# Kernel tuning notes

Hardware: AMD Instinct MI355X
Metric: run time of the kernel (lower is better)

Reference implementation:

```python
import jax, jax.numpy as jnp
import numpy as np

HEAD_SIZE = 128  # embeddings_dims // no_of_heads = 4096 // 32


def apply_rope(v):
    # v: [B, S, d] with d = HEAD_SIZE; interleaved-pair rotation as in source
    B, S, d = v.shape
    pos = jnp.arange(S, dtype=jnp.float32)[:, None]              # [S, 1]
    idx = jnp.arange(0, d, 2, dtype=jnp.float32)[None, :]        # [1, d//2]
    theta = jnp.power(10000.0, -2.0 * idx / d)                   # [1, d//2]
    angles = pos * theta                                         # [S, d//2]
    cos = jnp.cos(angles)
    sin = jnp.sin(angles)
    vr = v.reshape(B, S, d // 2, 2)
    x0, x1 = vr[..., 0], vr[..., 1]
    out = jnp.stack([x0 * cos - x1 * sin, x1 * cos + x0 * sin], axis=-1)
    return out.reshape(B, S, d)


def setup_inputs() -> dict:
    key = jax.random.key(0)
    kx, kq, kk, kv = jax.random.split(key, 4)
    B, S, D = 2, 4096, 4096
    d = HEAD_SIZE
    scale = 1.0 / np.sqrt(D)
    return {
        "x": jax.random.normal(kx, (B, S, D), dtype=jnp.float32),
        "Wq": jax.random.normal(kq, (d, D), dtype=jnp.float32) * scale,
        "Wk": jax.random.normal(kk, (d, D), dtype=jnp.float32) * scale,
        "Wv": jax.random.normal(kv, (d, D), dtype=jnp.float32) * scale,
    }


def reference(x, Wq, Wk, Wv):
    # single attention head, non-flash path (eval mode: dropout = identity)
    B, S, D = x.shape
    q = jnp.einsum('bsd,hd->bsh', x, Wq)  # [B, S, head]
    k = jnp.einsum('bsd,hd->bsh', x, Wk)
    v = jnp.einsum('bsd,hd->bsh', x, Wv)
    q = apply_rope(q)
    k = apply_rope(k)
    scale = k.shape[-1] ** (-0.5)
    scores = jnp.einsum('bqh,bkh->bqk', q, k) * scale  # [B, S, S]
    causal = jnp.tril(jnp.ones((S, S), dtype=bool))
    scores = jnp.where(causal, scores, -jnp.inf)
    weights = jax.nn.softmax(scores, axis=-1)
    out = jnp.einsum('bqk,bkh->bqh', weights, v)  # [B, S, head]
    return out
```

## Files before the change

### kernel.cpp

```cpp
#include <hip/hip_runtime.h>

typedef _Float16 half8 __attribute__((ext_vector_type(8)));
typedef _Float16 half2v __attribute__((ext_vector_type(2)));
typedef float f32x4 __attribute__((ext_vector_type(4)));

#define S_LEN 4096
#define D_DIM 4096
#define HD 128


__device__ __forceinline__ void gload_lds16(const _Float16* g, _Float16* l) {
    __builtin_amdgcn_global_load_lds(
        (const __attribute__((address_space(1))) unsigned int*)g,
        (__attribute__((address_space(3))) unsigned int*)l, 16, 0, 0);
}

__global__ __launch_bounds__(256) void convw_kernel(const float* __restrict__ wq,
                                                    const float* __restrict__ wk,
                                                    const float* __restrict__ wv,
                                                    _Float16* __restrict__ wh) {
    const int g = blockIdx.x * 256 + threadIdx.x;
    const int p = g >> 16;
    const int off = (g & 65535) * 8;
    const float* src = ((p == 0) ? wq : (p == 1) ? wk : wv) + off;
    float4 v0 = *(const float4*)src;
    float4 v1 = *(const float4*)(src + 4);
    half8 h = { (_Float16)v0.x, (_Float16)v0.y, (_Float16)v0.z, (_Float16)v0.w,
                (_Float16)v1.x, (_Float16)v1.y, (_Float16)v1.z, (_Float16)v1.w };
    *(half8*)&wh[(size_t)p * 524288 + off] = h;
}

#define QSTR 136
template<int KSPLIT>
__global__ __launch_bounds__(256) void proj_kernel(const float* __restrict__ x,
                                                   const _Float16* __restrict__ wh,
                                                   _Float16* __restrict__ qw,
                                                   _Float16* __restrict__ kw,
                                                   _Float16* __restrict__ vt,
                                                   float* __restrict__ P) {
    __shared__ __align__(16) _Float16 smem[17408];
    const int tid = threadIdx.x;
    const int wg = blockIdx.x;
    const int nwg = 384 * KSPLIT;
    const int swz = (wg & 7) * (nwg >> 3) + (wg >> 3);
    const int bx = swz % 3;
    const int rest = swz / 3;
    const int ks = (KSPLIT == 2) ? (rest & 1) : 0;
    const int M0 = ((KSPLIT == 2) ? (rest >> 1) : rest) * 64;
    const int NS = 128 / KSPLIT;
    const int lane = tid & 63, wv_ = tid >> 6;
    const int l15 = lane & 15, quad = lane >> 4;

    const int arow = tid >> 2, acol = (tid & 3) * 8;
    const float* xa = x + (size_t)(M0 + arow) * D_DIM + acol + ks * (D_DIM / 2);
    const _Float16* wsrc = wh + (size_t)bx * 128 * D_DIM + ks * (D_DIM / 2) +
                           (size_t)(wv_ * 32 + l15) * D_DIM + quad * 8;

    const int awoff = ((arow >> 4) * 64 + (arow & 15) + (tid & 3) * 16) * 8;
    const int rdoff = lane * 8;

    f32x4 acc[4][2];
    for (int mi = 0; mi < 4; ++mi)
        for (int ni = 0; ni < 2; ++ni)
            acc[mi][ni] = (f32x4){0.f, 0.f, 0.f, 0.f};

    auto stageA = [&](_Float16* buf, float4 A0, float4 A1) {
        half8 ha = { (_Float16)A0.x, (_Float16)A0.y, (_Float16)A0.z, (_Float16)A0.w,
                     (_Float16)A1.x, (_Float16)A1.y, (_Float16)A1.z, (_Float16)A1.w };
        *(half8*)&buf[awoff] = ha;
    };
    auto stageB = [&](_Float16* buf, int slab) {
        const _Float16* s = wsrc + slab * 32;
        gload_lds16(s,               &buf[2048 + wv_ * 1024]);
        gload_lds16(s + 16 * D_DIM,  &buf[2048 + wv_ * 1024 + 512]);
    };
    auto compute = [&](const _Float16* buf) {
        const _Float16* Af = buf + rdoff;
        const _Float16* Bf = buf + 2048 + wv_ * 1024 + rdoff;
        half8 af[4], bf[2];
        for (int mi = 0; mi < 4; ++mi)
            af[mi] = *(const half8*)(Af + mi * 512);
        for (int ni = 0; ni < 2; ++ni)
            bf[ni] = *(const half8*)(Bf + ni * 512);
        for (int mi = 0; mi < 4; ++mi)
            for (int ni = 0; ni < 2; ++ni)
                acc[mi][ni] = __builtin_amdgcn_mfma_f32_16x16x32_f16(af[mi], bf[ni],
                                                                     acc[mi][ni], 0, 0, 0);
    };

    float4 a0_0, a0_1, a1_0, a1_1;
    a0_0 = *(const float4*)(xa);      a0_1 = *(const float4*)(xa + 4);
    a1_0 = *(const float4*)(xa + 32); a1_1 = *(const float4*)(xa + 36);
    stageB(smem, 0);

    for (int i = 0; i < NS; i += 2) {
        stageA(smem, a0_0, a0_1);
        __syncthreads();
        if (i + 2 < NS) {
            a0_0 = *(const float4*)(xa + (i + 2) * 32);
            a0_1 = *(const float4*)(xa + (i + 2) * 32 + 4);
        }
        stageB(smem + 6144, i + 1);
        compute(smem);
        stageA(smem + 6144, a1_0, a1_1);
        __syncthreads();
        if (i + 3 < NS) {
            a1_0 = *(const float4*)(xa + (i + 3) * 32);
            a1_1 = *(const float4*)(xa + (i + 3) * 32 + 4);
        }
        if (i + 2 < NS) stageB(smem, i + 2);
        compute(smem + 6144);
    }
    __syncthreads();

    if (KSPLIT == 2) {
        float* sf = (float*)smem;
        for (int mi = 0; mi < 4; ++mi)
            for (int ni = 0; ni < 2; ++ni)
                for (int r = 0; r < 4; ++r)
                    sf[(mi * 16 + quad * 4 + r) * 132 + wv_ * 32 + ni * 16 + l15] =
                        acc[mi][ni][r];
        __syncthreads();
        const int row = tid >> 2, c0 = (tid & 3) * 32;
        float* dst = P + ((size_t)(ks * 3 + bx) * 8192 + M0 + row) * HD + c0;
        for (int j = 0; j < 8; ++j)
            *(float4*)(dst + j * 4) = *(const float4*)&sf[row * 132 + c0 + j * 4];
    } else if (bx < 2) {
        for (int mi = 0; mi < 4; ++mi)
            for (int ni = 0; ni < 2; ++ni)
                for (int r = 0; r < 4; ++r)
                    smem[(mi * 16 + quad * 4 + r) * QSTR + wv_ * 32 + ni * 16 + l15] =
                        (_Float16)acc[mi][ni][r];
        __syncthreads();
        _Float16* dst = ((bx == 0) ? qw : kw) + (size_t)M0 * HD;
        const int row = tid >> 2, c0 = (tid & 3) * 32;
        for (int j = 0; j < 4; ++j)
            *(half8*)&dst[row * HD + c0 + j * 8] = *(const half8*)&smem[row * QSTR + c0 + j * 8];
    } else {
        for (int mi = 0; mi < 4; ++mi)
            for (int ni = 0; ni < 2; ++ni)
                for (int r = 0; r < 4; ++r)
                    smem[(wv_ * 32 + ni * 16 + l15) * QSTR + mi * 16 + quad * 4 + r] =
                        (_Float16)acc[mi][ni][r];
        __syncthreads();
        _Float16* dst = vt + (size_t)(M0 >> 12) * HD * S_LEN + (M0 & (S_LEN - 1));
        const int hd = tid >> 1, s0 = (tid & 1) * 32;
        for (int j = 0; j < 4; ++j)
            *(half8*)&dst[(size_t)hd * S_LEN + s0 + j * 8] =
                *(const half8*)&smem[hd * QSTR + s0 + j * 8];
    }
}

__global__ __launch_bounds__(256) void combine_kernel(const float* __restrict__ P,
                                                      _Float16* __restrict__ qw,
                                                      _Float16* __restrict__ kw,
                                                      _Float16* __restrict__ vt) {
    const int tid = threadIdx.x;
    const int M0 = blockIdx.x * 64;
    const int row = tid >> 2, c0 = (tid & 3) * 32;
    if (blockIdx.y == 0) {
        const float* Pq0 = P + ((size_t)0 * 8192 + M0 + row) * HD + c0;
        const float* Pq1 = P + ((size_t)3 * 8192 + M0 + row) * HD + c0;
        const float* Pk0 = P + ((size_t)1 * 8192 + M0 + row) * HD + c0;
        const float* Pk1 = P + ((size_t)4 * 8192 + M0 + row) * HD + c0;
        float qv[32], kv[32];
#pragma unroll
        for (int j = 0; j < 8; ++j) {
            float4 a = *(const float4*)(Pq0 + j * 4);
            float4 b = *(const float4*)(Pq1 + j * 4);
            float4 c = *(const float4*)(Pk0 + j * 4);
            float4 d = *(const float4*)(Pk1 + j * 4);
            qv[j * 4 + 0] = a.x + b.x; qv[j * 4 + 1] = a.y + b.y;
            qv[j * 4 + 2] = a.z + b.z; qv[j * 4 + 3] = a.w + b.w;
            kv[j * 4 + 0] = c.x + d.x; kv[j * 4 + 1] = c.y + d.y;
            kv[j * 4 + 2] = c.z + d.z; kv[j * 4 + 3] = c.w + d.w;
        }
        const int s = (M0 + row) & (S_LEN - 1);
        half8 oq[4], ok[4];
#pragma unroll
        for (int jp = 0; jp < 16; ++jp) {
            const int pi = (c0 >> 1) + jp;
            const float theta = exp2f((float)pi * -0.4152410118609203f);
            float sn, cn;
            sincosf((float)s * theta, &sn, &cn);
            const float q0 = qv[2 * jp], q1 = qv[2 * jp + 1];
            const float k0 = kv[2 * jp], k1 = kv[2 * jp + 1];
            oq[jp >> 2][(2 * jp) & 7]     = (_Float16)(q0 * cn - q1 * sn);
            oq[jp >> 2][(2 * jp + 1) & 7] = (_Float16)(q1 * cn + q0 * sn);
            ok[jp >> 2][(2 * jp) & 7]     = (_Float16)(k0 * cn - k1 * sn);
            ok[jp >> 2][(2 * jp + 1) & 7] = (_Float16)(k1 * cn + k0 * sn);
        }
        _Float16* qdst = qw + (size_t)(M0 + row) * HD + c0;
        _Float16* kdst = kw + (size_t)(M0 + row) * HD + c0;
#pragma unroll
        for (int j = 0; j < 4; ++j) {
            *(half8*)(qdst + j * 8) = oq[j];
            *(half8*)(kdst + j * 8) = ok[j];
        }
    } else {
        __shared__ __align__(16) _Float16 sh[128][72];
        const float* Pv0 = P + ((size_t)2 * 8192 + M0 + row) * HD + c0;
        const float* Pv1 = P + ((size_t)5 * 8192 + M0 + row) * HD + c0;
#pragma unroll
        for (int j = 0; j < 8; ++j) {
            float4 a = *(const float4*)(Pv0 + j * 4);
            float4 b = *(const float4*)(Pv1 + j * 4);
            sh[c0 + j * 4 + 0][row] = (_Float16)(a.x + b.x);
            sh[c0 + j * 4 + 1][row] = (_Float16)(a.y + b.y);
            sh[c0 + j * 4 + 2][row] = (_Float16)(a.z + b.z);
            sh[c0 + j * 4 + 3][row] = (_Float16)(a.w + b.w);
        }
        __syncthreads();
        const int hd = tid >> 1, s0 = (tid & 1) * 32;
        _Float16* dst = vt + (size_t)(M0 >> 12) * HD * S_LEN + (size_t)hd * S_LEN +
                        (M0 & (S_LEN - 1)) + s0;
        for (int j = 0; j < 4; ++j)
            *(half8*)(dst + j * 8) = *(const half8*)&sh[hd][s0 + j * 8];
    }
}

__global__ __launch_bounds__(256) void rope_kernel(_Float16* __restrict__ qw,
                                                   _Float16* __restrict__ kw) {
    const int g = blockIdx.x * 256 + threadIdx.x;
    const int m = g >> 6, p = g & 63;
    const int s = m & (S_LEN - 1);
    const float theta = exp2f((float)p * -0.4152410118609203f);
    float sn, cn;
    sincosf((float)s * theta, &sn, &cn);
    const size_t off = (size_t)m * HD + 2 * p;
    half2v qv = *(half2v*)&qw[off];
    half2v kv = *(half2v*)&kw[off];
    float q0 = qv[0], q1 = qv[1], k0 = kv[0], k1 = kv[1];
    half2v qo = { (_Float16)(q0 * cn - q1 * sn), (_Float16)(q1 * cn + q0 * sn) };
    half2v ko = { (_Float16)(k0 * cn - k1 * sn), (_Float16)(k1 * cn + k0 * sn) };
    *(half2v*)&qw[off] = qo;
    *(half2v*)&kw[off] = ko;
}

__device__ __forceinline__ void load_kf(const _Float16* __restrict__ kb, int kbase,
                                        int l15, int quad, half8* kf) {
    const _Float16* kr = kb + (size_t)(kbase + l15) * HD + quad * 8;
    for (int kk = 0; kk < 4; ++kk) {
        kf[kk]     = *(const half8*)(kr + kk * 32);
        kf[4 + kk] = *(const half8*)(kr + 16 * HD + kk * 32);
    }
}

template<bool MASKED>
__device__ __forceinline__ void attn_tile(int kbase, int qg, int l15, int quad,
                                          const half8* kf,
                                          const _Float16* __restrict__ vtb,
                                          const half8* bq, f32x4* acc,
                                          float& mrun, float& lrun) {
    const float csc = 0.1275174348796053f;
    half8 va[8];
    const _Float16* vr = vtb + (size_t)l15 * S_LEN + kbase + quad * 8;
    for (int c = 0; c < 8; ++c)
        va[c] = *(const half8*)(vr + (size_t)c * 16 * S_LEN);
    f32x4 st0 = (f32x4){0.f, 0.f, 0.f, 0.f};
    f32x4 st1 = (f32x4){0.f, 0.f, 0.f, 0.f};
    for (int kk = 0; kk < 4; ++kk) {
        st0 = __builtin_amdgcn_mfma_f32_16x16x32_f16(kf[kk],     bq[kk], st0, 0, 0, 0);
        st1 = __builtin_amdgcn_mfma_f32_16x16x32_f16(kf[4 + kk], bq[kk], st1, 0, 0, 0);
    }
    float p0[4], p1[4];
    float mloc = -1e30f;
    for (int r = 0; r < 4; ++r) {
        float v0 = st0[r] * csc;
        float v1 = st1[r] * csc;
        if (MASKED) {
            const int key0 = kbase + quad * 4 + r;
            if (key0 > qg)      v0 = -1e30f;
            if (key0 + 16 > qg) v1 = -1e30f;
        }
        p0[r] = v0; p1[r] = v1;
        mloc = fmaxf(mloc, fmaxf(v0, v1));
    }
    mloc = fmaxf(mloc, __shfl_xor(mloc, 16));
    mloc = fmaxf(mloc, __shfl_xor(mloc, 32));
    const float mnew = fmaxf(mrun, mloc);
    const float alpha = exp2f(mrun - mnew);
    mrun = mnew;
    float ls = 0.f;
    for (int r = 0; r < 4; ++r) {
        p0[r] = exp2f(p0[r] - mnew);
        p1[r] = exp2f(p1[r] - mnew);
        ls += p0[r] + p1[r];
    }
    ls += __shfl_xor(ls, 16);
    ls += __shfl_xor(ls, 32);
    lrun = lrun * alpha + ls;
    for (int c = 0; c < 8; ++c)
        acc[c] *= alpha;
    int ph0 = __builtin_bit_cast(int, __builtin_amdgcn_cvt_pkrtz(p0[0], p0[1]));
    int ph1 = __builtin_bit_cast(int, __builtin_amdgcn_cvt_pkrtz(p0[2], p0[3]));
    int ph2 = __builtin_bit_cast(int, __builtin_amdgcn_cvt_pkrtz(p1[0], p1[1]));
    int ph3 = __builtin_bit_cast(int, __builtin_amdgcn_cvt_pkrtz(p1[2], p1[3]));
    const int s0 = (l15 + (((quad << 1)    ) & 3) * 16) * 4;
    const int s1 = (l15 + (((quad << 1) + 1) & 3) * 16) * 4;
    int a0 = __builtin_amdgcn_ds_bpermute(s0, ph0);
    int a1 = __builtin_amdgcn_ds_bpermute(s0, ph1);
    int a2 = __builtin_amdgcn_ds_bpermute(s1, ph0);
    int a3 = __builtin_amdgcn_ds_bpermute(s1, ph1);
    int b0 = __builtin_amdgcn_ds_bpermute(s0, ph2);
    int b1 = __builtin_amdgcn_ds_bpermute(s0, ph3);
    int b2 = __builtin_amdgcn_ds_bpermute(s1, ph2);
    int b3 = __builtin_amdgcn_ds_bpermute(s1, ph3);
    const bool lo = quad < 2;
    int4 pi = { lo ? a0 : b0, lo ? a1 : b1, lo ? a2 : b2, lo ? a3 : b3 };
    half8 pf = __builtin_bit_cast(half8, pi);
    for (int c = 0; c < 8; ++c)
        acc[c] = __builtin_amdgcn_mfma_f32_16x16x32_f16(va[c], pf, acc[c], 0, 0, 0);
}

__global__ __launch_bounds__(256) void attn_kernel(const _Float16* __restrict__ q,
                                                   const _Float16* __restrict__ k,
                                                   const _Float16* __restrict__ vt,
                                                   float* __restrict__ out) {
    __shared__ __align__(16) float Osh[4][16][132];
    __shared__ float msh[4][16];
    __shared__ float lsh[4][16];
    const int tid = threadIdx.x;
    const int lane = tid & 63, wv_ = tid >> 6;
    const int l15 = lane & 15, quad = lane >> 4;
    const int bidx = blockIdx.x;
    const int b = bidx & 1;
    const int t = 255 - (bidx >> 1);
    const int qb = t * 16;
    const int qg = qb + l15;

    const _Float16* qp = q + (size_t)(b * S_LEN + qb) * HD;
    half8 bq[4];
    for (int kk = 0; kk < 4; ++kk)
        bq[kk] = *(const half8*)&qp[l15 * HD + kk * 32 + quad * 8];

    f32x4 acc[8];
    for (int c = 0; c < 8; ++c) acc[c] = (f32x4){0.f, 0.f, 0.f, 0.f};
    float mrun = -1e30f, lrun = 0.f;

    const _Float16* kb = k + (size_t)b * S_LEN * HD;
    const _Float16* vtb = vt + (size_t)b * HD * S_LEN;

    const int nfull = (qb + 1) >> 5;
    const int kend = nfull * 32;
    const bool hasm = ((nfull & 3) == wv_);
    const int kb0 = wv_ * 32;

    half8 kf[8], kf2[8];
    if (kb0 < kend)      load_kf(kb, kb0, l15, quad, kf);
    else if (hasm)       load_kf(kb, kend, l15, quad, kf);
    for (int kbase = kb0; kbase < kend; kbase += 128) {
        const int kn = kbase + 128;
        if (kn < kend)   load_kf(kb, kn, l15, quad, kf2);
        else if (hasm)   load_kf(kb, kend, l15, quad, kf2);
        attn_tile<false>(kbase, qg, l15, quad, kf, vtb, bq, acc, mrun, lrun);
        for (int j = 0; j < 8; ++j) kf[j] = kf2[j];
    }
    if (hasm)
        attn_tile<true>(kend, qg, l15, quad, kf, vtb, bq, acc, mrun, lrun);

    for (int c = 0; c < 8; ++c)
        *(f32x4*)&Osh[wv_][l15][c * 16 + quad * 4] = acc[c];
    if (quad == 0) { msh[wv_][l15] = mrun; lsh[wv_][l15] = lrun; }
    __syncthreads();

    const int qr = tid >> 4, dg = (tid & 15) * 8;
    float m0 = msh[0][qr], m1 = msh[1][qr], m2 = msh[2][qr], m3 = msh[3][qr];
    float mm = fmaxf(fmaxf(m0, m1), fmaxf(m2, m3));
    float f0 = exp2f(m0 - mm), f1 = exp2f(m1 - mm), f2 = exp2f(m2 - mm), f3 = exp2f(m3 - mm);
    float l = lsh[0][qr] * f0 + lsh[1][qr] * f1 + lsh[2][qr] * f2 + lsh[3][qr] * f3;
    f32x4 oa = (f32x4){0.f, 0.f, 0.f, 0.f}, ob = oa;
    oa += *(f32x4*)&Osh[0][qr][dg] * f0;  ob += *(f32x4*)&Osh[0][qr][dg + 4] * f0;
    oa += *(f32x4*)&Osh[1][qr][dg] * f1;  ob += *(f32x4*)&Osh[1][qr][dg + 4] * f1;
    oa += *(f32x4*)&Osh[2][qr][dg] * f2;  ob += *(f32x4*)&Osh[2][qr][dg + 4] * f2;
    oa += *(f32x4*)&Osh[3][qr][dg] * f3;  ob += *(f32x4*)&Osh[3][qr][dg + 4] * f3;
    const float inv = 1.0f / l;
    float* op = out + (size_t)(b * S_LEN + qb + qr) * HD + dg;
    *(float4*)op       = (float4){oa[0] * inv, oa[1] * inv, oa[2] * inv, oa[3] * inv};
    *(float4*)(op + 4) = (float4){ob[0] * inv, ob[1] * inv, ob[2] * inv, ob[3] * inv};
}

extern "C" void kernel_launch(void* const* d_in, const int* in_sizes, int n_in,
                              void* d_out, int out_size, void* d_ws, size_t ws_size,
                              hipStream_t stream) {
    const float* x  = (const float*)d_in[0];
    const float* Wq = (const float*)d_in[1];
    const float* Wk = (const float*)d_in[2];
    const float* Wv = (const float*)d_in[3];
    float* out = (float*)d_out;
    char* ws = (char*)d_ws;
    _Float16* qw = (_Float16*)(ws);
    _Float16* kw = (_Float16*)(ws + (2u << 20));
    _Float16* vt = (_Float16*)(ws + (4u << 20));
    _Float16* wh = (_Float16*)(ws + (6u << 20));
    float* P = (float*)(ws + (9u << 20));

    const size_t need2 = (size_t)(9u << 20) + (size_t)2 * 3 * 8192 * 128 * 4;
    convw_kernel<<<dim3(768), dim3(256), 0, stream>>>(Wq, Wk, Wv, wh);
    if (ws_size >= need2) {
        proj_kernel<2><<<dim3(768), dim3(256), 0, stream>>>(x, wh, qw, kw, vt, P);
        combine_kernel<<<dim3(128, 2), dim3(256), 0, stream>>>(P, qw, kw, vt);
    } else {
        proj_kernel<1><<<dim3(384), dim3(256), 0, stream>>>(x, wh, qw, kw, vt, P);
        rope_kernel<<<dim3(2048), dim3(256), 0, stream>>>(qw, kw);
    }
    attn_kernel<<<dim3(512), dim3(256), 0, stream>>>(qw, kw, vt, out);
}
```

Measured before the change: 343.4 us.

## Pre-convert x to fp16 and use direct-to-LDS projection GEMM

Adds a kernel that converts x and the weights to fp16 in one pass, then a new projection kernel that loads both A and B tiles with global-to-LDS async loads, double-buffered, with 64-wide k steps. This removes register-based fp32 loading and conversion of x inside the GEMM. In exchange it adds an extra full pass over x (read fp32, write fp16) and needs a larger workspace; it falls back to the old path otherwise.

Result: slower. 373.4 us (+8.7%).

```diff
diff --git a/kernel.cpp b/kernel.cpp
--- a/kernel.cpp
+++ b/kernel.cpp
@@ -13,6 +13,33 @@
     __builtin_amdgcn_global_load_lds(
         (const __attribute__((address_space(1))) unsigned int*)g,
         (__attribute__((address_space(3))) unsigned int*)l, 16, 0, 0);
+}
+
+__global__ __launch_bounds__(256) void convx_kernel(const float* __restrict__ x,
+                                                    const float* __restrict__ wq,
+                                                    const float* __restrict__ wk,
+                                                    const float* __restrict__ wv,
+                                                    _Float16* __restrict__ xh,
+                                                    _Float16* __restrict__ wh) {
+    const int g = blockIdx.x * 256 + threadIdx.x;
+    const float* src;
+    _Float16* dst;
+    if (g < 4194304) {
+        const int off = g * 8;
+        src = x + off;
+        dst = xh + off;
+    } else {
+        const int h = g - 4194304;
+        const int p = h >> 16;
+        const int off = (h & 65535) * 8;
+        src = ((p == 0) ? wq : (p == 1) ? wk : wv) + off;
+        dst = wh + (size_t)p * 524288 + off;
+    }
+    float4 v0 = *(const float4*)src;
+    float4 v1 = *(const float4*)(src + 4);
+    half8 hv = { (_Float16)v0.x, (_Float16)v0.y, (_Float16)v0.z, (_Float16)v0.w,
+                 (_Float16)v1.x, (_Float16)v1.y, (_Float16)v1.z, (_Float16)v1.w };
+    *(half8*)dst = hv;
 }
 
 __global__ __launch_bounds__(256) void convw_kernel(const float* __restrict__ wq,
@@ -28,6 +55,77 @@
     half8 h = { (_Float16)v0.x, (_Float16)v0.y, (_Float16)v0.z, (_Float16)v0.w,
                 (_Float16)v1.x, (_Float16)v1.y, (_Float16)v1.z, (_Float16)v1.w };
     *(half8*)&wh[(size_t)p * 524288 + off] = h;
+}
+
+__global__ __launch_bounds__(256) void projd_kernel(const _Float16* __restrict__ xh,
+                                                    const _Float16* __restrict__ wh,
+                                                    float* __restrict__ P) {
+    __shared__ __align__(16) _Float16 smem[24576];
+    const int tid = threadIdx.x;
+    const int wg = blockIdx.x;
+    const int swz = (wg & 7) * 96 + (wg >> 3);
+    const int bx = swz % 3;
+    const int rest = swz / 3;
+    const int ks = rest & 1;
+    const int M0 = (rest >> 1) * 64;
+    const int lane = tid & 63, wv_ = tid >> 6;
+    const int l15 = lane & 15, quad = lane >> 4;
+
+    const _Float16* asrc = xh + (size_t)(M0 + wv_ * 16 + l15) * D_DIM + ks * (D_DIM / 2) + quad * 8;
+    const _Float16* bsrc = wh + (size_t)bx * 524288 +
+                           (size_t)(wv_ * 32 + l15) * D_DIM + ks * (D_DIM / 2) + quad * 8;
+
+    f32x4 acc[4][2];
+    for (int mi = 0; mi < 4; ++mi)
+        for (int ni = 0; ni < 2; ++ni)
+            acc[mi][ni] = (f32x4){0.f, 0.f, 0.f, 0.f};
+
+    auto stage = [&](int bufsel, int p) {
+        _Float16* buf = smem + bufsel * 12288;
+        const _Float16* a = asrc + p * 64;
+        gload_lds16(a,      buf + (wv_ * 2 + 0) * 512);
+        gload_lds16(a + 32, buf + (wv_ * 2 + 1) * 512);
+        const _Float16* b = bsrc + p * 64;
+        gload_lds16(b,                buf + 4096 + ((wv_ * 2 + 0) * 2 + 0) * 512);
+        gload_lds16(b + 32,           buf + 4096 + ((wv_ * 2 + 0) * 2 + 1) * 512);
+        gload_lds16(b + 16 * D_DIM,   buf + 4096 + ((wv_ * 2 + 1) * 2 + 0) * 512);
+        gload_lds16(b + 16 * D_DIM + 32, buf + 4096 + ((wv_ * 2 + 1) * 2 + 1) * 512);
+    };
+    auto compute = [&](int bufsel) {
+        const _Float16* buf = smem + bufsel * 12288 + lane * 8;
+        half8 af[4][2], bf[2][2];
+        for (int mi = 0; mi < 4; ++mi)
+            for (int kk = 0; kk < 2; ++kk)
+                af[mi][kk] = *(const half8*)(buf + (mi * 2 + kk) * 512);
+        for (int ni = 0; ni < 2; ++ni)
+            for (int kk = 0; kk < 2; ++kk)
+                bf[ni][kk] = *(const half8*)(buf + 4096 + ((wv_ * 2 + ni) * 2 + kk) * 512);
+        for (int kk = 0; kk < 2; ++kk)
+            for (int mi = 0; mi < 4; ++mi)
+                for (int ni = 0; ni < 2; ++ni)
+                    acc[mi][ni] = __builtin_amdgcn_mfma_f32_16x16x32_f16(af[mi][kk], bf[ni][kk],
+                                                                         acc[mi][ni], 0, 0, 0);
+    };
+
+    stage(0, 0);
+    for (int p = 0; p < 32; ++p) {
+        __syncthreads();
+        if (p + 1 < 32) stage((p + 1) & 1, p + 1);
+        compute(p & 1);
+    }
+    __syncthreads();
+
+    float* sf = (float*)smem;
+    for (int mi = 0; mi < 4; ++mi)
+        for (int ni = 0; ni < 2; ++ni)
+            for (int r = 0; r < 4; ++r)
+                sf[(mi * 16 + quad * 4 + r) * 132 + wv_ * 32 + ni * 16 + l15] =
+                    acc[mi][ni][r];
+    __syncthreads();
+    const int row = tid >> 2, c0 = (tid & 3) * 32;
+    float* dst = P + ((size_t)(ks * 3 + bx) * 8192 + M0 + row) * HD + c0;
+    for (int j = 0; j < 8; ++j)
+        *(float4*)(dst + j * 4) = *(const float4*)&sf[row * 132 + c0 + j * 4];
 }
 
 #define QSTR 136
@@ -55,7 +153,6 @@
     const float* xa = x + (size_t)(M0 + arow) * D_DIM + acol + ks * (D_DIM / 2);
     const _Float16* wsrc = wh + (size_t)bx * 128 * D_DIM + ks * (D_DIM / 2) +
                            (size_t)(wv_ * 32 + l15) * D_DIM + quad * 8;
-
     const int awoff = ((arow >> 4) * 64 + (arow & 15) + (tid & 3) * 16) * 8;
     const int rdoff = lane * 8;
 
@@ -71,8 +168,8 @@
     };
     auto stageB = [&](_Float16* buf, int slab) {
         const _Float16* s = wsrc + slab * 32;
-        gload_lds16(s,               &buf[2048 + wv_ * 1024]);
-        gload_lds16(s + 16 * D_DIM,  &buf[2048 + wv_ * 1024 + 512]);
+        gload_lds16(s,              &buf[2048 + wv_ * 1024]);
+        gload_lds16(s + 16 * D_DIM, &buf[2048 + wv_ * 1024 + 512]);
     };
     auto compute = [&](const _Float16* buf) {
         const _Float16* Af = buf + rdoff;
@@ -394,13 +491,20 @@
     _Float16* vt = (_Float16*)(ws + (4u << 20));
     _Float16* wh = (_Float16*)(ws + (6u << 20));
     float* P = (float*)(ws + (9u << 20));
+    _Float16* xh = (_Float16*)(ws + (33u << 20));
 
     const size_t need2 = (size_t)(9u << 20) + (size_t)2 * 3 * 8192 * 128 * 4;
-    convw_kernel<<<dim3(768), dim3(256), 0, stream>>>(Wq, Wk, Wv, wh);
-    if (ws_size >= need2) {
+    const size_t need3 = (size_t)(33u << 20) + (size_t)8192 * 4096 * 2;
+    if (ws_size >= need3) {
+        convx_kernel<<<dim3(17152), dim3(256), 0, stream>>>(x, Wq, Wk, Wv, xh, wh);
+        projd_kernel<<<dim3(768), dim3(256), 0, stream>>>(xh, wh, P);
+        combine_kernel<<<dim3(128, 2), dim3(256), 0, stream>>>(P, qw, kw, vt);
+    } else if (ws_size >= need2) {
+        convw_kernel<<<dim3(768), dim3(256), 0, stream>>>(Wq, Wk, Wv, wh);
         proj_kernel<2><<<dim3(768), dim3(256), 0, stream>>>(x, wh, qw, kw, vt, P);
         combine_kernel<<<dim3(128, 2), dim3(256), 0, stream>>>(P, qw, kw, vt);
     } else {
+        convw_kernel<<<dim3(768), dim3(256), 0, stream>>>(Wq, Wk, Wv, wh);
         proj_kernel<1><<<dim3(384), dim3(256), 0, stream>>>(x, wh, qw, kw, vt, P);
         rope_kernel<<<dim3(2048), dim3(256), 0, stream>>>(qw, kw);
     }
```

## Split attention KV range across two blocks with separate merge kernel

Applied to the files above, without the earlier changes.

Replaces the single attention kernel with a split-KV version: each query tile's causal key range is divided into two halves handled by separate workgroups, which write partial max, sum and output to workspace. A merge kernel then rescales and combines the eight per-wave partials into the final output. This doubles the grid so more CUs stay busy on the unbalanced causal workload, at the cost of an extra launch and the partial-output traffic through global memory. It falls back to the old kernel when the workspace is too small.

After: 349.0 us. No clear change (+1.7%).

```diff
diff --git a/kernel.cpp b/kernel.cpp
--- a/kernel.cpp
+++ b/kernel.cpp
@@ -55,7 +55,6 @@
     const float* xa = x + (size_t)(M0 + arow) * D_DIM + acol + ks * (D_DIM / 2);
     const _Float16* wsrc = wh + (size_t)bx * 128 * D_DIM + ks * (D_DIM / 2) +
                            (size_t)(wv_ * 32 + l15) * D_DIM + quad * 8;
-
     const int awoff = ((arow >> 4) * 64 + (arow & 15) + (tid & 3) * 16) * 8;
     const int rdoff = lane * 8;
 
@@ -71,8 +70,8 @@
     };
     auto stageB = [&](_Float16* buf, int slab) {
         const _Float16* s = wsrc + slab * 32;
-        gload_lds16(s,               &buf[2048 + wv_ * 1024]);
-        gload_lds16(s + 16 * D_DIM,  &buf[2048 + wv_ * 1024 + 512]);
+        gload_lds16(s,              &buf[2048 + wv_ * 1024]);
+        gload_lds16(s + 16 * D_DIM, &buf[2048 + wv_ * 1024 + 512]);
     };
     auto compute = [&](const _Float16* buf) {
         const _Float16* Af = buf + rdoff;
@@ -313,6 +312,102 @@
         acc[c] = __builtin_amdgcn_mfma_f32_16x16x32_f16(va[c], pf, acc[c], 0, 0, 0);
 }
 
+__global__ __launch_bounds__(256, 4) void attn_split(const _Float16* __restrict__ q,
+                                                     const _Float16* __restrict__ k,
+                                                     const _Float16* __restrict__ vt,
+                                                     float* __restrict__ Pm,
+                                                     float* __restrict__ Pl,
+                                                     float* __restrict__ Po) {
+    const int tid = threadIdx.x;
+    const int lane = tid & 63, wv_ = tid >> 6;
+    const int l15 = lane & 15, quad = lane >> 4;
+    const int bidx = blockIdx.x;
+    const int b = bidx & 1;
+    const int rest = bidx >> 1;
+    const int t = 255 - (rest >> 1);
+    const int h = rest & 1;
+    const int qb = t * 16;
+    const int qg = qb + l15;
+
+    const _Float16* qp = q + (size_t)(b * S_LEN + qb) * HD;
+    half8 bq[4];
+    for (int kk = 0; kk < 4; ++kk)
+        bq[kk] = *(const half8*)&qp[l15 * HD + kk * 32 + quad * 8];
+
+    f32x4 acc[8];
+    for (int c = 0; c < 8; ++c) acc[c] = (f32x4){0.f, 0.f, 0.f, 0.f};
+    float mrun = -1e30f, lrun = 0.f;
+
+    const _Float16* kb = k + (size_t)b * S_LEN * HD;
+    const _Float16* vtb = vt + (size_t)b * HD * S_LEN;
+
+    const int nfull = (qb + 1) >> 5;
+    const int n0 = nfull >> 1;
+    const int istart = h ? n0 : 0;
+    const int iend   = h ? nfull : n0;
+    const bool hasm = h && (((iend - istart) & 3) == wv_);
+
+    int idx = istart + wv_;
+    half8 kf[8], kf2[8];
+    if (idx < iend)      load_kf(kb, idx * 32, l15, quad, kf);
+    else if (hasm)       load_kf(kb, nfull * 32, l15, quad, kf);
+    for (; idx < iend; idx += 4) {
+        const int nx = idx + 4;
+        if (nx < iend)   load_kf(kb, nx * 32, l15, quad, kf2);
+        else if (hasm)   load_kf(kb, nfull * 32, l15, quad, kf2);
+        attn_tile<false>(idx * 32, qg, l15, quad, kf, vtb, bq, acc, mrun, lrun);
+        for (int j = 0; j < 8; ++j) kf[j] = kf2[j];
+    }
+    if (hasm)
+        attn_tile<true>(nfull * 32, qg, l15, quad, kf, vtb, bq, acc, mrun, lrun);
+
+    const int pidx = bidx * 4 + wv_;
+    float* po = Po + ((size_t)pidx * 16 + l15) * HD + quad * 4;
+    for (int c = 0; c < 8; ++c)
+        *(f32x4*)(po + c * 16) = acc[c];
+    if (quad == 0) {
+        Pm[pidx * 16 + l15] = mrun;
+        Pl[pidx * 16 + l15] = lrun;
+    }
+}
+
+__global__ __launch_bounds__(256) void attn_merge(const float* __restrict__ Pm,
+                                                  const float* __restrict__ Pl,
+                                                  const float* __restrict__ Po,
+                                                  float* __restrict__ out) {
+    const int tid = threadIdx.x;
+    const int cidx = blockIdx.x;
+    const int b = cidx & 1;
+    const int t = cidx >> 1;
+    const int qb = t * 16;
+    const int qr = tid >> 4, dg = (tid & 15) * 8;
+    const int rest0 = (255 - t) * 2;
+    float m[8], l[8];
+    float mm = -1e30f;
+#pragma unroll
+    for (int i = 0; i < 8; ++i) {
+        const int pidx = ((rest0 + (i >> 2)) * 2 + b) * 4 + (i & 3);
+        m[i] = Pm[pidx * 16 + qr];
+        l[i] = Pl[pidx * 16 + qr];
+        mm = fmaxf(mm, m[i]);
+    }
+    float ls = 0.f;
+    f32x4 oa = (f32x4){0.f, 0.f, 0.f, 0.f}, ob = oa;
+#pragma unroll
+    for (int i = 0; i < 8; ++i) {
+        const int pidx = ((rest0 + (i >> 2)) * 2 + b) * 4 + (i & 3);
+        const float f = exp2f(m[i] - mm);
+        ls += l[i] * f;
+        const float* p = Po + ((size_t)pidx * 16 + qr) * HD + dg;
+        oa += *(const f32x4*)p * f;
+        ob += *(const f32x4*)(p + 4) * f;
+    }
+    const float inv = 1.0f / ls;
+    float* op = out + (size_t)(b * S_LEN + qb + qr) * HD + dg;
+    *(float4*)op       = (float4){oa[0] * inv, oa[1] * inv, oa[2] * inv, oa[3] * inv};
+    *(float4*)(op + 4) = (float4){ob[0] * inv, ob[1] * inv, ob[2] * inv, ob[3] * inv};
+}
+
 __global__ __launch_bounds__(256) void attn_kernel(const _Float16* __restrict__ q,
                                                    const _Float16* __restrict__ k,
                                                    const _Float16* __restrict__ vt,
@@ -393,9 +488,14 @@
     _Float16* kw = (_Float16*)(ws + (2u << 20));
     _Float16* vt = (_Float16*)(ws + (4u << 20));
     _Float16* wh = (_Float16*)(ws + (6u << 20));
-    float* P = (float*)(ws + (9u << 20));
+    float* P  = (float*)(ws + (9u << 20));
+    float* Po = (float*)(ws + (33u << 20));
+    float* Pm = (float*)(ws + (65u << 20));
+    float* Pl = (float*)(ws + (65u << 20) + (256u << 10));
 
     const size_t need2 = (size_t)(9u << 20) + (size_t)2 * 3 * 8192 * 128 * 4;
+    const size_t needA = (size_t)(65u << 20) + (512u << 10);
+
     convw_kernel<<<dim3(768), dim3(256), 0, stream>>>(Wq, Wk, Wv, wh);
     if (ws_size >= need2) {
         proj_kernel<2><<<dim3(768), dim3(256), 0, stream>>>(x, wh, qw, kw, vt, P);
@@ -404,5 +504,10 @@
         proj_kernel<1><<<dim3(384), dim3(256), 0, stream>>>(x, wh, qw, kw, vt, P);
         rope_kernel<<<dim3(2048), dim3(256), 0, stream>>>(qw, kw);
     }
-    attn_kernel<<<dim3(512), dim3(256), 0, stream>>>(qw, kw, vt, out);
-}
+    if (ws_size >= needA) {
+        attn_split<<<dim3(1024), dim3(256), 0, stream>>>(qw, kw, vt, Pm, Pl, Po);
+        attn_merge<<<dim3(512), dim3(256), 0, stream>>>(Pm, Pl, Po, out);
+    } else {
+        attn_kernel<<<dim3(512), dim3(256), 0, stream>>>(qw, kw, vt, out);
+    }
+}
```

## Use 64-wide K slabs in split-K projection and precompute RoPE trig table

Applied to the files above, without the earlier changes.

Adds a dedicated split-K projection kernel that stages 64-element K slabs per iteration instead of 32. This halves the number of barriers and pipeline steps and doubles the MFMA work between syncs, at the cost of more LDS and registers (launch bounds now target 3 blocks per CU). It also moves the RoPE sin/cos evaluation into a small separate kernel that writes a cos/sin table, which the combine kernel then reads instead of computing sincosf per element. The table adds an extra launch and a 2 MB workspace buffer, and it requires more workspace before the fast path is taken.

New measurement: 349.5 us. About the same (+1.8%).

```diff
diff --git a/kernel.cpp b/kernel.cpp
--- a/kernel.cpp
+++ b/kernel.cpp
@@ -30,32 +30,134 @@
     *(half8*)&wh[(size_t)p * 524288 + off] = h;
 }
 
+__global__ __launch_bounds__(256) void trig_kernel(float* __restrict__ tab) {
+    const int g = blockIdx.x * 256 + threadIdx.x;
+    const int s = g >> 6, p = g & 63;
+    const float theta = exp2f((float)p * -0.4152410118609203f);
+    float sn, cn;
+    sincosf((float)s * theta, &sn, &cn);
+    *(float2*)&tab[g * 2] = (float2){cn, sn};
+}
+
+__global__ __launch_bounds__(256, 3) void proj64_kernel(const float* __restrict__ x,
+                                                        const _Float16* __restrict__ wh,
+                                                        float* __restrict__ P) {
+    __shared__ __align__(16) _Float16 smem[24576];
+    const int tid = threadIdx.x;
+    const int wg = blockIdx.x;
+    const int swz = (wg & 7) * 96 + (wg >> 3);
+    const int bx = swz % 3;
+    const int rest = swz / 3;
+    const int ks = rest & 1;
+    const int M0 = (rest >> 1) * 64;
+    const int lane = tid & 63, wv_ = tid >> 6;
+    const int l15 = lane & 15, quad = lane >> 4;
+
+    const int arow = tid >> 2, acol = (tid & 3) * 16;
+    const float* xa = x + (size_t)(M0 + arow) * D_DIM + acol + ks * (D_DIM / 2);
+    const int c8a = (tid & 3) * 2;
+    const int awoff0 = (((arow >> 4) * 2 + (c8a >> 2)) * 64 + (arow & 15) + (c8a & 3) * 16) * 8;
+    const int c8b = c8a + 1;
+    const int awoff1 = (((arow >> 4) * 2 + (c8b >> 2)) * 64 + (arow & 15) + (c8b & 3) * 16) * 8;
+
+    const _Float16* wsrc = wh + (size_t)bx * 524288 + ks * (D_DIM / 2) +
+                           (size_t)(wv_ * 32 + l15) * D_DIM + quad * 8;
+
+    f32x4 acc[4][2];
+    for (int mi = 0; mi < 4; ++mi)
+        for (int ni = 0; ni < 2; ++ni)
+            acc[mi][ni] = (f32x4){0.f, 0.f, 0.f, 0.f};
+
+    auto stageA = [&](_Float16* buf, float4 A0, float4 A1, float4 A2, float4 A3) {
+        half8 h0 = { (_Float16)A0.x, (_Float16)A0.y, (_Float16)A0.z, (_Float16)A0.w,
+                     (_Float16)A1.x, (_Float16)A1.y, (_Float16)A1.z, (_Float16)A1.w };
+        half8 h1 = { (_Float16)A2.x, (_Float16)A2.y, (_Float16)A2.z, (_Float16)A2.w,
+                     (_Float16)A3.x, (_Float16)A3.y, (_Float16)A3.z, (_Float16)A3.w };
+        *(half8*)&buf[awoff0] = h0;
+        *(half8*)&buf[awoff1] = h1;
+    };
+    auto stageB = [&](_Float16* buf, int p) {
+        const _Float16* s = wsrc + p * 64;
+        gload_lds16(s,                     &buf[4096 + ((wv_ * 2 + 0) * 2 + 0) * 512]);
+        gload_lds16(s + 32,                &buf[4096 + ((wv_ * 2 + 0) * 2 + 1) * 512]);
+        gload_lds16(s + 16 * D_DIM,        &buf[4096 + ((wv_ * 2 + 1) * 2 + 0) * 512]);
+        gload_lds16(s + 16 * D_DIM + 32,   &buf[4096 + ((wv_ * 2 + 1) * 2 + 1) * 512]);
+    };
+    auto compute = [&](const _Float16* buf) {
+        const _Float16* Af = buf + lane * 8;
+        const _Float16* Bf = buf + 4096 + wv_ * 2048 + lane * 8;
+        half8 af[4][2], bf[2][2];
+        for (int mi = 0; mi < 4; ++mi)
+            for (int kk = 0; kk < 2; ++kk)
+                af[mi][kk] = *(const half8*)(Af + (mi * 2 + kk) * 512);
+        for (int ni = 0; ni < 2; ++ni)
+            for (int kk = 0; kk < 2; ++kk)
+                bf[ni][kk] = *(const half8*)(Bf + (ni * 2 + kk) * 512);
+        for (int kk = 0; kk < 2; ++kk)
+            for (int mi = 0; mi < 4; ++mi)
+                for (int ni = 0; ni < 2; ++ni)
+                    acc[mi][ni] = __builtin_amdgcn_mfma_f32_16x16x32_f16(af[mi][kk], bf[ni][kk],
+                                                                         acc[mi][ni], 0, 0, 0);
+    };
+
+#define LOADA(R0, R1, R2, R3, p)                           \
+    R0 = *(const float4*)(xa + (p) * 64);                  \
+    R1 = *(const float4*)(xa + (p) * 64 + 4);              \
+    R2 = *(const float4*)(xa + (p) * 64 + 8);              \
+    R3 = *(const float4*)(xa + (p) * 64 + 12);
+
+    float4 aA0, aA1, aA2, aA3, aB0, aB1, aB2, aB3;
+    LOADA(aA0, aA1, aA2, aA3, 0)
+    LOADA(aB0, aB1, aB2, aB3, 1)
+    stageB(smem, 0);
+
+    for (int p = 0; p < 32; p += 2) {
+        stageA(smem, aA0, aA1, aA2, aA3);
+        __syncthreads();
+        if (p + 2 < 32) { LOADA(aA0, aA1, aA2, aA3, p + 2) }
+        stageB(smem + 12288, p + 1);
+        compute(smem);
+        stageA(smem + 12288, aB0, aB1, aB2, aB3);
+        __syncthreads();
+        if (p + 3 < 32) { LOADA(aB0, aB1, aB2, aB3, p + 3) }
+        if (p + 2 < 32) stageB(smem, p + 2);
+        compute(smem + 12288);
+    }
+#undef LOADA
+    __syncthreads();
+
+    float* sf = (float*)smem;
+    for (int mi = 0; mi < 4; ++mi)
+        for (int ni = 0; ni < 2; ++ni)
+            for (int r = 0; r < 4; ++r)
+                sf[(mi * 16 + quad * 4 + r) * 132 + wv_ * 32 + ni * 16 + l15] =
+                    acc[mi][ni][r];
+    __syncthreads();
+    const int row = tid >> 2, c0 = (tid & 3) * 32;
+    float* dst = P + ((size_t)(ks * 3 + bx) * 8192 + M0 + row) * HD + c0;
+    for (int j = 0; j < 8; ++j)
+        *(float4*)(dst + j * 4) = *(const float4*)&sf[row * 132 + c0 + j * 4];
+}
+
 #define QSTR 136
-template<int KSPLIT>
 __global__ __launch_bounds__(256) void proj_kernel(const float* __restrict__ x,
                                                    const _Float16* __restrict__ wh,
                                                    _Float16* __restrict__ qw,
                                                    _Float16* __restrict__ kw,
-                                                   _Float16* __restrict__ vt,
-                                                   float* __restrict__ P) {
+                                                   _Float16* __restrict__ vt) {
     __shared__ __align__(16) _Float16 smem[17408];
     const int tid = threadIdx.x;
     const int wg = blockIdx.x;
-    const int nwg = 384 * KSPLIT;
-    const int swz = (wg & 7) * (nwg >> 3) + (wg >> 3);
+    const int swz = (wg & 7) * 48 + (wg >> 3);
     const int bx = swz % 3;
-    const int rest = swz / 3;
-    const int ks = (KSPLIT == 2) ? (rest & 1) : 0;
-    const int M0 = ((KSPLIT == 2) ? (rest >> 1) : rest) * 64;
-    const int NS = 128 / KSPLIT;
+    const int M0 = (swz / 3) * 64;
     const int lane = tid & 63, wv_ = tid >> 6;
     const int l15 = lane & 15, quad = lane >> 4;
 
     const int arow = tid >> 2, acol = (tid & 3) * 8;
-    const float* xa = x + (size_t)(M0 + arow) * D_DIM + acol + ks * (D_DIM / 2);
-    const _Float16* wsrc = wh + (size_t)bx * 128 * D_DIM + ks * (D_DIM / 2) +
+    const float* xa = x + (size_t)(M0 + arow) * D_DIM + acol;
+    const _Float16* wsrc = wh + (size_t)bx * 128 * D_DIM +
                            (size_t)(wv_ * 32 + l15) * D_DIM + quad * 8;
-
     const int awoff = ((arow >> 4) * 64 + (arow & 15) + (tid & 3) * 16) * 8;
     const int rdoff = lane * 8;
 
@@ -71,8 +173,8 @@
     };
     auto stageB = [&](_Float16* buf, int slab) {
         const _Float16* s = wsrc + slab * 32;
-        gload_lds16(s,               &buf[2048 + wv_ * 1024]);
-        gload_lds16(s + 16 * D_DIM,  &buf[2048 + wv_ * 1024 + 512]);
+        gload_lds16(s,              &buf[2048 + wv_ * 1024]);
+        gload_lds16(s + 16 * D_DIM, &buf[2048 + wv_ * 1024 + 512]);
     };
     auto compute = [&](const _Float16* buf) {
         const _Float16* Af = buf + rdoff;
@@ -93,10 +195,10 @@
     a1_0 = *(const float4*)(xa + 32); a1_1 = *(const float4*)(xa + 36);
     stageB(smem, 0);
 
-    for (int i = 0; i < NS; i += 2) {
+    for (int i = 0; i < 128; i += 2) {
         stageA(smem, a0_0, a0_1);
         __syncthreads();
-        if (i + 2 < NS) {
+        if (i + 2 < 128) {
             a0_0 = *(const float4*)(xa + (i + 2) * 32);
             a0_1 = *(const float4*)(xa + (i + 2) * 32 + 4);
         }
@@ -104,28 +206,16 @@
         compute(smem);
         stageA(smem + 6144, a1_0, a1_1);
         __syncthreads();
-        if (i + 3 < NS) {
+        if (i + 3 < 128) {
             a1_0 = *(const float4*)(xa + (i + 3) * 32);
             a1_1 = *(const float4*)(xa + (i + 3) * 32 + 4);
         }
-        if (i + 2 < NS) stageB(smem, i + 2);
+        if (i + 2 < 128) stageB(smem, i + 2);
         compute(smem + 6144);
     }
     __syncthreads();
 
-    if (KSPLIT == 2) {
-        float* sf = (float*)smem;
-        for (int mi = 0; mi < 4; ++mi)
-            for (int ni = 0; ni < 2; ++ni)
-                for (int r = 0; r < 4; ++r)
-                    sf[(mi * 16 + quad * 4 + r) * 132 + wv_ * 32 + ni * 16 + l15] =
-                        acc[mi][ni][r];
-        __syncthreads();
-        const int row = tid >> 2, c0 = (tid & 3) * 32;
-        float* dst = P + ((size_t)(ks * 3 + bx) * 8192 + M0 + row) * HD + c0;
-        for (int j = 0; j < 8; ++j)
-            *(float4*)(dst + j * 4) = *(const float4*)&sf[row * 132 + c0 + j * 4];
-    } else if (bx < 2) {
+    if (bx < 2) {
         for (int mi = 0; mi < 4; ++mi)
             for (int ni = 0; ni < 2; ++ni)
                 for (int r = 0; r < 4; ++r)
@@ -152,6 +242,7 @@
 }
 
 __global__ __launch_bounds__(256) void combine_kernel(const float* __restrict__ P,
+                                                      const float* __restrict__ tab,
                                                       _Float16* __restrict__ qw,
                                                       _Float16* __restrict__ kw,
                                                       _Float16* __restrict__ vt) {
@@ -176,13 +267,12 @@
             kv[j * 4 + 2] = c.z + d.z; kv[j * 4 + 3] = c.w + d.w;
         }
         const int s = (M0 + row) & (S_LEN - 1);
+        const float2* tb = (const float2*)tab + s * 64 + (c0 >> 1);
         half8 oq[4], ok[4];
 #pragma unroll
         for (int jp = 0; jp < 16; ++jp) {
-            const int pi = (c0 >> 1) + jp;
-            const float theta = exp2f((float)pi * -0.4152410118609203f);
-            float sn, cn;
-            sincosf((float)s * theta, &sn, &cn);
+            const float2 cs = tb[jp];
+            const float cn = cs.x, sn = cs.y;
             const float q0 = qv[2 * jp], q1 = qv[2 * jp + 1];
             const float k0 = kv[2 * jp], k1 = kv[2 * jp + 1];
             oq[jp >> 2][(2 * jp) & 7]     = (_Float16)(q0 * cn - q1 * sn);
@@ -393,15 +483,17 @@
     _Float16* kw = (_Float16*)(ws + (2u << 20));
     _Float16* vt = (_Float16*)(ws + (4u << 20));
     _Float16* wh = (_Float16*)(ws + (6u << 20));
-    float* P = (float*)(ws + (9u << 20));
-
-    const size_t need2 = (size_t)(9u << 20) + (size_t)2 * 3 * 8192 * 128 * 4;
+    float* P   = (float*)(ws + (9u << 20));
+    float* tab = (float*)(ws + (33u << 20));
+
+    const size_t need = (size_t)(35u << 20);
     convw_kernel<<<dim3(768), dim3(256), 0, stream>>>(Wq, Wk, Wv, wh);
-    if (ws_size >= need2) {
-        proj_kernel<2><<<dim3(768), dim3(256), 0, stream>>>(x, wh, qw, kw, vt, P);
-        combine_kernel<<<dim3(128, 2), dim3(256), 0, stream>>>(P, qw, kw, vt);
+    if (ws_size >= need) {
+        trig_kernel<<<dim3(1024), dim3(256), 0, stream>>>(tab);
+        proj64_kernel<<<dim3(768), dim3(256), 0, stream>>>(x, wh, P);
+        combine_kernel<<<dim3(128, 2), dim3(256), 0, stream>>>(P, tab, qw, kw, vt);
     } else {
-        proj_kernel<1><<<dim3(384), dim3(256), 0, stream>>>(x, wh, qw, kw, vt, P);
+        proj_kernel<<<dim3(384), dim3(256), 0, stream>>>(x, wh, qw, kw, vt);
         rope_kernel<<<dim3(2048), dim3(256), 0, stream>>>(qw, kw);
     }
     attn_kernel<<<dim3(512), dim3(256), 0, stream>>>(qw, kw, vt, out);
```
